# Kernel tuning notes

Measured on AMD Instinct MI355X. Metric: run time of the kernel, lower is better.

The kernel has to match this reference:

```python
import jax, jax.numpy as jnp
import numpy as np

E, D, A, EMB, V = 2048, 512, 512, 512, 10000  # encoder_dim, decoder_dim, attention_dim, embed_dim, vocab


def setup_inputs() -> dict:
    key = jax.random.key(0)
    ks = jax.random.split(key, 20)
    s = 0.02
    B, P, T = 64, 196, 40
    return {
        "encoder_out": jax.random.normal(ks[0], (B, P, E), jnp.float32),
        "captions": jax.random.randint(ks[1], (B, T), 0, V),
        "caption_lengths": jax.random.randint(ks[2], (B,), 1, T),
        "enc_att_W": jax.random.normal(ks[3], (E, A)) * s,
        "enc_att_b": jnp.zeros((A,)),
        "dec_att_W": jax.random.normal(ks[4], (D, A)) * s,
        "dec_att_b": jnp.zeros((A,)),
        "full_att_W": jax.random.normal(ks[5], (A,)) * s,
        "full_att_b": jnp.zeros(()),
        "embedding": jax.random.normal(ks[6], (V, EMB)) * s,
        "W_ih": jax.random.normal(ks[7], (EMB + E, 4 * D)) * s,
        "b_ih": jnp.zeros((4 * D,)),
        "W_hh": jax.random.normal(ks[8], (D, 4 * D)) * s,
        "b_hh": jnp.zeros((4 * D,)),
        "init_h_W": jax.random.normal(ks[9], (E, D)) * s,
        "init_h_b": jnp.zeros((D,)),
        "init_c_W": jax.random.normal(ks[10], (E, D)) * s,
        "init_c_b": jnp.zeros((D,)),
        "fc_W": jax.random.normal(ks[11], (D, V)) * s,
        "fc_b": jnp.zeros((V,)),
        "f_beta_W": jax.random.normal(ks[12], (D, E)) * s,
        "f_beta_b": jnp.zeros((E,)),
    }


def reference(encoder_out, captions, caption_lengths,
              enc_att_W, enc_att_b, dec_att_W, dec_att_b, full_att_W, full_att_b,
              embedding, W_ih, b_ih, W_hh, b_hh,
              init_h_W, init_h_b, init_c_W, init_c_b,
              fc_W, fc_b, f_beta_W, f_beta_b):
    # init hidden state from mean-pooled encoder features
    mean_enc = encoder_out.mean(axis=1)                      # [B, E]
    h = mean_enc @ init_h_W + init_h_b                       # [B, D]
    c = mean_enc @ init_c_W + init_c_b

    embs = embedding[captions]                               # [B, T, EMB]
    # encoder_att(encoder_out) is step-invariant -> precompute once
    att1 = jnp.einsum('bpe,ea->bpa', encoder_out, enc_att_W) + enc_att_b  # [B, P, A]

    def step(carry, emb_t):
        h, c = carry
        att2 = h @ dec_att_W + dec_att_b                     # [B, A]
        e = jax.nn.relu(att1 + att2[:, None, :]) @ full_att_W + full_att_b  # [B, P]
        alpha = jax.nn.softmax(e, axis=1)                    # [B, P]
        context = jnp.einsum('bpe,bp->be', encoder_out, alpha)  # [B, E]
        gate = jax.nn.sigmoid(h @ f_beta_W + f_beta_b)       # [B, E]
        x = jnp.concatenate([emb_t, gate * context], axis=1)  # [B, EMB+E]
        gates = x @ W_ih + b_ih + h @ W_hh + b_hh            # [B, 4D]
        i, f, g, o = jnp.split(gates, 4, axis=1)
        c_new = jax.nn.sigmoid(f) * c + jax.nn.sigmoid(i) * jnp.tanh(g)
        h_new = jax.nn.sigmoid(o) * jnp.tanh(c_new)
        preds = h_new @ fc_W + fc_b                          # [B, V] (dropout = identity at eval)
        return (h_new, c_new), (preds, alpha)

    (_, _), (preds_t, alphas_t) = jax.lax.scan(step, (h, c), jnp.swapaxes(embs, 0, 1))
    predictions = jnp.swapaxes(preds_t, 0, 1)                # [B, T, V]
    alphas = jnp.swapaxes(alphas_t, 0, 1)                    # [B, T, P]
    return predictions, alphas
```

## Files before the change

kernel.cpp:

```cpp
#include <hip/hip_runtime.h>
#include <cstdint>
#include <cstddef>

#define B_   64
#define P_   196
#define E_   2048
#define A_   512
#define D_   512
#define EMB_ 512
#define V_   10000
#define T_   40
#define NCAT  4608
#define VPAD  10112

typedef unsigned short u16;
typedef __attribute__((ext_vector_type(8))) short bf16x8;
typedef __attribute__((ext_vector_type(4))) float f32x4;

__device__ __forceinline__ f32x4 mfma_bf16(bf16x8 a, bf16x8 b, f32x4 c) {
  return __builtin_amdgcn_mfma_f32_16x16x32_bf16(a, b, c, 0, 0, 0);
}
__device__ __forceinline__ u16 f2b(float f) {
  unsigned u = __builtin_bit_cast(unsigned, f);
  u += 0x7fffu + ((u >> 16) & 1u);
  return (u16)(u >> 16);
}
__device__ __forceinline__ float b2f(u16 s) {
  unsigned u = ((unsigned)s) << 16;
  return __builtin_bit_cast(float, u);
}
__device__ __forceinline__ float sigf(float x) { return 1.0f / (1.0f + __expf(-x)); }

__device__ __forceinline__ void gl_lds16(const u16* gsrc, u16* ldst) {
  __builtin_amdgcn_global_load_lds(
      (const __attribute__((address_space(1))) unsigned int*)gsrc,
      (__attribute__((address_space(3))) unsigned int*)ldst,
      16, 0, 0);
}

__global__ __launch_bounds__(256) void k_cvt_bf16(const float* __restrict__ s,
                                                  u16* __restrict__ d, int n4) {
  int i = blockIdx.x * 256 + threadIdx.x;
  if (i >= n4) return;
  float4 v = reinterpret_cast<const float4*>(s)[i];
  u16* o = d + (size_t)i * 4;
  o[0] = f2b(v.x); o[1] = f2b(v.y); o[2] = f2b(v.z); o[3] = f2b(v.w);
}

__global__ __launch_bounds__(256) void k_mean(const float* __restrict__ enc,
                                              u16* __restrict__ meanE_bf) {
  int i = blockIdx.x * 256 + threadIdx.x;
  int b = i >> 11, e = i & 2047;
  const float* p = enc + (size_t)b * P_ * E_ + e;
  float s = 0.f;
  for (int pp = 0; pp < P_; ++pp) s += p[(size_t)pp * E_];
  meanE_bf[i] = f2b(s * (1.0f / (float)P_));
}

__global__ __launch_bounds__(256) void k_transpose_bf16(
    const float* __restrict__ src, int srcStride,
    u16* __restrict__ dst, int dstStride, int N, int K) {
  __shared__ float t[32][33];
  int kt = blockIdx.x * 32, nt = blockIdx.y * 32;
  int tx = threadIdx.x & 31, ty = threadIdx.x >> 5;
  #pragma unroll
  for (int i = 0; i < 4; ++i) {
    int k = kt + ty + i * 8, n = nt + tx;
    t[ty + i * 8][tx] = (k < K && n < N) ? src[(size_t)k * srcStride + n] : 0.0f;
  }
  __syncthreads();
  #pragma unroll
  for (int i = 0; i < 4; ++i) {
    int n = nt + ty + i * 8, k = kt + tx;
    if (n < N && k < K) dst[(size_t)n * dstStride + k] = f2b(t[tx][ty + i * 8]);
  }
}

__global__ __launch_bounds__(256) void k_emb(const int* __restrict__ captions,
                                             const float* __restrict__ embedding,
                                             u16* __restrict__ embs) {
  int i = blockIdx.x * 256 + threadIdx.x;
  int m = i >> 9, k = i & 511;
  int t = m >> 6, b = m & 63;
  int cap = captions[b * T_ + t];
  embs[i] = f2b(embedding[(size_t)cap * EMB_ + k]);
}

__global__ __launch_bounds__(256) void k_bsum(const float* __restrict__ a,
                                              const float* __restrict__ b,
                                              float* __restrict__ o) {
  int i = blockIdx.x * 256 + threadIdx.x;
  o[i] = a[i] + b[i];
}

__global__ __launch_bounds__(256) void k_catbias(const float* __restrict__ hb,
                                                 const float* __restrict__ cb,
                                                 float* __restrict__ o) {
  int i = blockIdx.x * 256 + threadIdx.x;
  o[i] = (i < 512) ? hb[i] : cb[i - 512];
}

__global__ __launch_bounds__(256) void k_hc_pack(const float* __restrict__ initHC,
                                                 u16* __restrict__ h0_bf,
                                                 float* __restrict__ c_f) {
  int i = blockIdx.x * 256 + threadIdx.x;
  int b = i >> 9, d = i & 511;
  h0_bf[i] = f2b(initHC[b * 1024 + d]);
  c_f[i]  = initHC[b * 1024 + 512 + d];
}

template <bool BF16OUT>
__global__ __launch_bounds__(256) void k_gemm_bt(
    const u16* __restrict__ Am, const u16* __restrict__ Bt,
    const float* __restrict__ bias, void* __restrict__ outp, int K, int N) {
  int m0 = blockIdx.x * 64, n0 = blockIdx.y * 64;
  int w = threadIdx.x >> 6, lane = threadIdx.x & 63;
  int lr = lane & 15, lg = lane >> 4;
  const u16* ap = Am + (size_t)(m0 + 16 * w + lr) * K + lg * 8;
  const u16* bp = Bt + (size_t)(n0 + lr) * K + lg * 8;
  f32x4 acc0 = {}, acc1 = {}, acc2 = {}, acc3 = {};
  for (int k = 0; k < K; k += 32) {
    bf16x8 a  = *reinterpret_cast<const bf16x8*>(ap + k);
    bf16x8 b0 = *reinterpret_cast<const bf16x8*>(bp + k);
    bf16x8 b1 = *reinterpret_cast<const bf16x8*>(bp + (size_t)16 * K + k);
    bf16x8 b2 = *reinterpret_cast<const bf16x8*>(bp + (size_t)32 * K + k);
    bf16x8 b3 = *reinterpret_cast<const bf16x8*>(bp + (size_t)48 * K + k);
    acc0 = mfma_bf16(a, b0, acc0);
    acc1 = mfma_bf16(a, b1, acc1);
    acc2 = mfma_bf16(a, b2, acc2);
    acc3 = mfma_bf16(a, b3, acc3);
  }
  int row = m0 + 16 * w + 4 * lg;
  f32x4 accs[4] = {acc0, acc1, acc2, acc3};
  #pragma unroll
  for (int ns = 0; ns < 4; ++ns) {
    int col = n0 + 16 * ns + lr;
    float bv = bias[col];
    #pragma unroll
    for (int r = 0; r < 4; ++r) {
      float v = accs[ns][r] + bv;
      if (BF16OUT) ((u16*)outp)[(size_t)(row + r) * N + col] = f2b(v);
      else         ((float*)outp)[(size_t)(row + r) * N + col] = v;
    }
  }
}

template <bool BF16OUT>
__global__ __launch_bounds__(256) void k_gemm128(
    const u16* __restrict__ Am, const u16* __restrict__ Bt,
    const float* __restrict__ bias, void* __restrict__ outp, int K, int N) {
  __shared__ u16 lA[128 * 64];
  __shared__ u16 lB[128 * 64];
  int n0 = blockIdx.x * 128, m0 = blockIdx.y * 128;
  int w = threadIdx.x >> 6, lane = threadIdx.x & 63;
  int wr = w >> 1, wc = w & 1;
  int lr = lane & 15, lg = lane >> 4;
  int srow = lane >> 3;
  int scol = (lane & 7) * 8;
  f32x4 acc[4][4] = {};
  for (int kt = 0; kt < K; kt += 64) {
    #pragma unroll
    for (int q = 0; q < 4; ++q) {
      int r = (w * 4 + q) * 8 + srow;
      gl_lds16(Am + (size_t)(m0 + r) * K + kt + scol, &lA[(w * 4 + q) * 512]);
      gl_lds16(Bt + (size_t)(n0 + r) * K + kt + scol, &lB[(w * 4 + q) * 512]);
    }
    __syncthreads();
    #pragma unroll
    for (int kk = 0; kk < 2; ++kk) {
      bf16x8 af[4], bf[4];
      #pragma unroll
      for (int m = 0; m < 4; ++m)
        af[m] = *reinterpret_cast<const bf16x8*>(&lA[(wr * 64 + m * 16 + lr) * 64 + kk * 32 + lg * 8]);
      #pragma unroll
      for (int n = 0; n < 4; ++n)
        bf[n] = *reinterpret_cast<const bf16x8*>(&lB[(wc * 64 + n * 16 + lr) * 64 + kk * 32 + lg * 8]);
      #pragma unroll
      for (int m = 0; m < 4; ++m)
        #pragma unroll
        for (int n = 0; n < 4; ++n)
          acc[m][n] = mfma_bf16(af[m], bf[n], acc[m][n]);
    }
    __syncthreads();
  }
  #pragma unroll
  for (int n = 0; n < 4; ++n) {
    int col = n0 + wc * 64 + n * 16 + lr;
    float bv = bias[col];
    #pragma unroll
    for (int m = 0; m < 4; ++m) {
      int row = m0 + wr * 64 + m * 16 + lg * 4;
      #pragma unroll
      for (int r = 0; r < 4; ++r) {
        float v = acc[m][n][r] + bv;
        if (BF16OUT) ((u16*)outp)[(size_t)(row + r) * N + col] = f2b(v);
        else         ((float*)outp)[(size_t)(row + r) * N + col] = v;
      }
    }
  }
}

__global__ __launch_bounds__(256) void k_gemm_fc(
    const u16* __restrict__ Hall1, const u16* __restrict__ fcWT,
    const float* __restrict__ fc_b, float* __restrict__ preds_out) {
  __shared__ u16 lA[128 * 64];
  __shared__ u16 lB[128 * 64];
  int n0 = blockIdx.x * 128, m0 = blockIdx.y * 128;
  int w = threadIdx.x >> 6, lane = threadIdx.x & 63;
  int wr = w >> 1, wc = w & 1;
  int lr = lane & 15, lg = lane >> 4;
  int srow = lane >> 3;
  int scol = (lane & 7) * 8;
  f32x4 acc[4][4] = {};
  for (int kt = 0; kt < 512; kt += 64) {
    #pragma unroll
    for (int q = 0; q < 4; ++q) {
      int r = (w * 4 + q) * 8 + srow;
      gl_lds16(Hall1 + (size_t)(m0 + r) * 512 + kt + scol, &lA[(w * 4 + q) * 512]);
      gl_lds16(fcWT + (size_t)(n0 + r) * 512 + kt + scol, &lB[(w * 4 + q) * 512]);
    }
    __syncthreads();
    #pragma unroll
    for (int kk = 0; kk < 2; ++kk) {
      bf16x8 af[4], bf[4];
      #pragma unroll
      for (int m = 0; m < 4; ++m)
        af[m] = *reinterpret_cast<const bf16x8*>(&lA[(wr * 64 + m * 16 + lr) * 64 + kk * 32 + lg * 8]);
      #pragma unroll
      for (int n = 0; n < 4; ++n)
        bf[n] = *reinterpret_cast<const bf16x8*>(&lB[(wc * 64 + n * 16 + lr) * 64 + kk * 32 + lg * 8]);
      #pragma unroll
      for (int m = 0; m < 4; ++m)
        #pragma unroll
        for (int n = 0; n < 4; ++n)
          acc[m][n] = mfma_bf16(af[m], bf[n], acc[m][n]);
    }
    __syncthreads();
  }
  #pragma unroll
  for (int n = 0; n < 4; ++n) {
    int col = n0 + wc * 64 + n * 16 + lr;
    if (col >= V_) continue;
    float bv = fc_b[col];
    #pragma unroll
    for (int m = 0; m < 4; ++m) {
      int row = m0 + wr * 64 + m * 16 + lg * 4;
      #pragma unroll
      for (int r = 0; r < 4; ++r) {
        int rr = row + r;
        int t = rr >> 6, b = rr & 63;
        preds_out[((size_t)b * T_ + t) * V_ + col] = acc[m][n][r] + bv;
      }
    }
  }
}

__global__ __launch_bounds__(256) void k_stepA(
    const u16* __restrict__ h_bf, const u16* __restrict__ catW,
    const float* __restrict__ dec_b, const float* __restrict__ fbeta_b,
    const float* __restrict__ embW_t,
    float* __restrict__ att2, float* __restrict__ gate,
    float* __restrict__ gates) {
  int n0 = blockIdx.x * 64;
  int w = threadIdx.x >> 6, lane = threadIdx.x & 63;
  int lr = lane & 15, lg = lane >> 4;
  const u16* ap = h_bf + (size_t)(16 * w + lr) * 512 + lg * 8;
  const u16* bp = catW + (size_t)(n0 + lr) * 512 + lg * 8;
  f32x4 acc0 = {}, acc1 = {}, acc2 = {}, acc3 = {};
  for (int k = 0; k < 512; k += 32) {
    bf16x8 a  = *reinterpret_cast<const bf16x8*>(ap + k);
    bf16x8 b0 = *reinterpret_cast<const bf16x8*>(bp + k);
    bf16x8 b1 = *reinterpret_cast<const bf16x8*>(bp + (size_t)16 * 512 + k);
    bf16x8 b2 = *reinterpret_cast<const bf16x8*>(bp + (size_t)32 * 512 + k);
    bf16x8 b3 = *reinterpret_cast<const bf16x8*>(bp + (size_t)48 * 512 + k);
    acc0 = mfma_bf16(a, b0, acc0);
    acc1 = mfma_bf16(a, b1, acc1);
    acc2 = mfma_bf16(a, b2, acc2);
    acc3 = mfma_bf16(a, b3, acc3);
  }
  int brow = 16 * w + 4 * lg;
  f32x4 accs[4] = {acc0, acc1, acc2, acc3};
  #pragma unroll
  for (int ns = 0; ns < 4; ++ns) {
    int n = n0 + 16 * ns + lr;
    #pragma unroll
    for (int r = 0; r < 4; ++r) {
      int b = brow + r;
      float v = accs[ns][r];
      if (n < 512) {
        att2[b * 512 + n] = v + dec_b[n];
      } else if (n < 2560) {
        int j = n - 512;
        gate[b * 2048 + j] = sigf(v + fbeta_b[j]);
      } else {
        int j = n - 2560;
        gates[b * 2048 + j] = v + embW_t[b * 2048 + j];
      }
    }
  }
}

__global__ __launch_bounds__(256) void k_stepB(
    const u16* __restrict__ att1, const float* __restrict__ att2,
    const float* __restrict__ wf, const float* __restrict__ bf_,
    float* __restrict__ e) {
  int unit = blockIdx.x * 4 + (threadIdx.x >> 6);
  int lane = threadIdx.x & 63;
  int b = unit / 196;
  const u16*  a1  = att1 + (size_t)unit * 512 + lane * 8;
  const float* a2 = att2 + b * 512 + lane * 8;
  const float* wv = wf + lane * 8;
  float s = 0.f;
  #pragma unroll
  for (int j = 0; j < 8; ++j) {
    float x = b2f(a1[j]) + a2[j];
    s += fmaxf(x, 0.f) * wv[j];
  }
  #pragma unroll
  for (int off = 32; off > 0; off >>= 1) s += __shfl_xor(s, off);
  if (lane == 0) e[unit] = s + bf_[0];
}

__global__ __launch_bounds__(256) void k_stepD(
    const float* __restrict__ e, const u16* __restrict__ enc_bf,
    const float* __restrict__ gate, float* __restrict__ alphas,
    u16* __restrict__ gctx) {
  __shared__ float sal[P_];
  __shared__ float red[256];
  int b = blockIdx.x >> 3, ch = blockIdx.x & 7;
  int tid = threadIdx.x;
  float ev = (tid < P_) ? e[b * P_ + tid] : -1e30f;
  red[tid] = ev; __syncthreads();
  for (int s = 128; s > 0; s >>= 1) {
    if (tid < s) red[tid] = fmaxf(red[tid], red[tid + s]);
    __syncthreads();
  }
  float mx = red[0]; __syncthreads();
  float ex = (tid < P_) ? __expf(ev - mx) : 0.f;
  red[tid] = ex; __syncthreads();
  for (int s = 128; s > 0; s >>= 1) {
    if (tid < s) red[tid] += red[tid + s];
    __syncthreads();
  }
  float inv = 1.0f / red[0];
  if (tid < P_) {
    float al = ex * inv;
    sal[tid] = al;
    if (ch == 0) alphas[(size_t)b * (T_ * P_) + tid] = al;
  }
  __syncthreads();
  int eidx = ch * 256 + tid;
  const u16* ep = enc_bf + (size_t)b * P_ * E_ + eidx;
  float acc = 0.f;
  #pragma unroll 4
  for (int p = 0; p < P_; ++p) acc += sal[p] * b2f(ep[(size_t)p * E_]);
  gctx[b * E_ + eidx] = f2b(acc * gate[b * E_ + eidx]);
}

__global__ __launch_bounds__(256) void k_stepE1(
    const u16* __restrict__ gctx, const u16* __restrict__ Wt,
    float* __restrict__ gates) {
  int n0 = (blockIdx.x & 31) * 64;
  int k0 = (blockIdx.x >> 5) * 256;
  int w = threadIdx.x >> 6, lane = threadIdx.x & 63;
  int lr = lane & 15, lg = lane >> 4;
  const u16* ap = gctx + (size_t)(16 * w + lr) * 2048 + lg * 8 + k0;
  const u16* bp = Wt + (size_t)(n0 + lr) * 2048 + lg * 8 + k0;
  f32x4 acc0 = {}, acc1 = {}, acc2 = {}, acc3 = {};
  for (int k = 0; k < 256; k += 32) {
    bf16x8 a  = *reinterpret_cast<const bf16x8*>(ap + k);
    bf16x8 b0 = *reinterpret_cast<const bf16x8*>(bp + k);
    bf16x8 b1 = *reinterpret_cast<const bf16x8*>(bp + (size_t)16 * 2048 + k);
    bf16x8 b2 = *reinterpret_cast<const bf16x8*>(bp + (size_t)32 * 2048 + k);
    bf16x8 b3 = *reinterpret_cast<const bf16x8*>(bp + (size_t)48 * 2048 + k);
    acc0 = mfma_bf16(a, b0, acc0);
    acc1 = mfma_bf16(a, b1, acc1);
    acc2 = mfma_bf16(a, b2, acc2);
    acc3 = mfma_bf16(a, b3, acc3);
  }
  int brow = 16 * w + 4 * lg;
  f32x4 accs[4] = {acc0, acc1, acc2, acc3};
  #pragma unroll
  for (int ns = 0; ns < 4; ++ns) {
    int n = n0 + 16 * ns + lr;
    #pragma unroll
    for (int r = 0; r < 4; ++r)
      atomicAdd(&gates[(brow + r) * 2048 + n], accs[ns][r]);
  }
}

__global__ __launch_bounds__(256) void k_stepE2(
    const float* __restrict__ gates, float* __restrict__ c, u16* __restrict__ h_out) {
  int i = blockIdx.x * 256 + threadIdx.x;
  int b = i >> 9, d = i & 511;
  const float* g = gates + (size_t)b * 2048;
  float gi = g[d], gf = g[d + 512], gg = g[d + 1024], go = g[d + 1536];
  float cn = sigf(gf) * c[i] + sigf(gi) * tanhf(gg);
  float hn = sigf(go) * tanhf(cn);
  c[i] = cn;
  h_out[i] = f2b(hn);
}

extern "C" void kernel_launch(void* const* d_in, const int* in_sizes, int n_in,
                              void* d_out, int out_size, void* d_ws, size_t ws_size,
                              hipStream_t stream) {
  (void)in_sizes; (void)n_in; (void)out_size;
  const float* enc        = (const float*)d_in[0];
  const int*   captions   = (const int*)d_in[1];
  const float* enc_att_W  = (const float*)d_in[3];
  const float* enc_att_b  = (const float*)d_in[4];
  const float* dec_att_W  = (const float*)d_in[5];
  const float* dec_att_b  = (const float*)d_in[6];
  const float* full_att_W = (const float*)d_in[7];
  const float* full_att_b = (const float*)d_in[8];
  const float* embedding  = (const float*)d_in[9];
  const float* W_ih       = (const float*)d_in[10];
  const float* b_ih       = (const float*)d_in[11];
  const float* W_hh       = (const float*)d_in[12];
  const float* b_hh       = (const float*)d_in[13];
  const float* init_h_W   = (const float*)d_in[14];
  const float* init_h_b   = (const float*)d_in[15];
  const float* init_c_W   = (const float*)d_in[16];
  const float* init_c_b   = (const float*)d_in[17];
  const float* fc_W       = (const float*)d_in[18];
  const float* fc_b       = (const float*)d_in[19];
  const float* f_beta_W   = (const float*)d_in[20];
  const float* f_beta_b   = (const float*)d_in[21];

  float* preds_out  = (float*)d_out;
  float* alphas_out = (float*)d_out + (size_t)B_ * T_ * V_;

  char* w = (char*)d_ws;
  auto alloc = [&](size_t bytes) -> char* {
    char* p = w; w += (bytes + 255) & ~(size_t)255; return p;
  };
  u16*   enc_bf   = (u16*)  alloc((size_t)B_ * P_ * E_ * 2);
  u16*   att1_bf  = (u16*)  alloc((size_t)B_ * P_ * A_ * 2);
  u16*   catW     = (u16*)  alloc((size_t)NCAT * 512 * 2);
  u16*   fcWT     = (u16*)  alloc((size_t)VPAD * 512 * 2);
  u16*   encattWT = (u16*)  alloc((size_t)A_ * E_ * 2);
  u16*   WihembT  = (u16*)  alloc((size_t)2048 * 512 * 2);
  u16*   Wih2T    = (u16*)  alloc((size_t)2048 * 2048 * 2);
  u16*   embs_bf  = (u16*)  alloc((size_t)T_ * B_ * EMB_ * 2);
  float* embW     = (float*)alloc((size_t)T_ * B_ * 2048 * 4);
  u16*   Hall     = (u16*)  alloc((size_t)(T_ + 1) * B_ * D_ * 2);
  u16*   catInit  = (u16*)  alloc((size_t)1024 * 2048 * 2);
  float* catInitB = (float*)alloc(1024 * 4);
  float* initHC   = (float*)alloc((size_t)B_ * 1024 * 4);
  u16*   meanE_bf = (u16*)  alloc((size_t)B_ * E_ * 2);
  float* c_f      = (float*)alloc((size_t)B_ * D_ * 4);
  float* att2_f   = (float*)alloc((size_t)B_ * A_ * 4);
  float* gate_f   = (float*)alloc((size_t)B_ * E_ * 4);
  float* gates_f  = (float*)alloc((size_t)B_ * 2048 * 4);
  float* e_f      = (float*)alloc((size_t)B_ * P_ * 4);
  u16*   gctx_bf  = (u16*)  alloc((size_t)B_ * E_ * 2);
  float* bsum     = (float*)alloc(2048 * 4);
  if ((size_t)(w - (char*)d_ws) > ws_size) return;

  k_cvt_bf16<<<25088, 256, 0, stream>>>(enc, enc_bf, (B_ * P_ * E_) / 4);
  k_mean<<<512, 256, 0, stream>>>(enc, meanE_bf);
  k_transpose_bf16<<<dim3(16, 16), 256, 0, stream>>>(dec_att_W, 512, catW, 512, 512, 512);
  k_transpose_bf16<<<dim3(16, 64), 256, 0, stream>>>(f_beta_W, 2048, catW + (size_t)512 * 512, 512, 2048, 512);
  k_transpose_bf16<<<dim3(16, 64), 256, 0, stream>>>(W_hh, 2048, catW + (size_t)2560 * 512, 512, 2048, 512);
  hipMemsetAsync(fcWT + (size_t)V_ * 512, 0, (size_t)(VPAD - V_) * 512 * 2, stream);
  k_transpose_bf16<<<dim3(16, 313), 256, 0, stream>>>(fc_W, 10000, fcWT, 512, 10000, 512);
  k_transpose_bf16<<<dim3(64, 16), 256, 0, stream>>>(enc_att_W, 512, encattWT, 2048, 512, 2048);
  k_transpose_bf16<<<dim3(16, 64), 256, 0, stream>>>(W_ih, 2048, WihembT, 512, 2048, 512);
  k_transpose_bf16<<<dim3(64, 64), 256, 0, stream>>>(W_ih + (size_t)512 * 2048, 2048, Wih2T, 2048, 2048, 2048);
  k_transpose_bf16<<<dim3(64, 16), 256, 0, stream>>>(init_h_W, 512, catInit, 2048, 512, 2048);
  k_transpose_bf16<<<dim3(64, 16), 256, 0, stream>>>(init_c_W, 512, catInit + (size_t)512 * 2048, 2048, 512, 2048);
  k_catbias<<<4, 256, 0, stream>>>(init_h_b, init_c_b, catInitB);
  k_bsum<<<8, 256, 0, stream>>>(b_ih, b_hh, bsum);
  k_emb<<<5120, 256, 0, stream>>>(captions, embedding, embs_bf);
  k_gemm_bt<false><<<dim3(1, 16), 256, 0, stream>>>(meanE_bf, catInit, catInitB, initHC, 2048, 1024);
  k_hc_pack<<<128, 256, 0, stream>>>(initHC, Hall, c_f);
  k_gemm128<true><<<dim3(4, 98), 256, 0, stream>>>(enc_bf, encattWT, enc_att_b, att1_bf, 2048, 512);
  k_gemm128<false><<<dim3(16, 20), 256, 0, stream>>>(embs_bf, WihembT, bsum, embW, 512, 2048);

  for (int t = 0; t < T_; ++t) {
    const u16* h_prev = Hall + (size_t)t * B_ * D_;
    u16* h_next = Hall + (size_t)(t + 1) * B_ * D_;
    k_stepA<<<NCAT / 64, 256, 0, stream>>>(h_prev, catW, dec_att_b, f_beta_b,
                                           embW + (size_t)t * B_ * 2048,
                                           att2_f, gate_f, gates_f);
    k_stepB<<<3136, 256, 0, stream>>>(att1_bf, att2_f, full_att_W, full_att_b, e_f);
    k_stepD<<<512, 256, 0, stream>>>(e_f, enc_bf, gate_f, alphas_out + (size_t)t * P_, gctx_bf);
    k_stepE1<<<256, 256, 0, stream>>>(gctx_bf, Wih2T, gates_f);
    k_stepE2<<<128, 256, 0, stream>>>(gates_f, c_f, h_next);
  }
  k_gemm_fc<<<dim3(VPAD / 128, (T_ * B_) / 128), 256, 0, stream>>>(
      Hall + (size_t)B_ * D_, fcWT, fc_b, preds_out);
}
```

Before: 2.555 ms.

## Fuse recurrent step kernels into one persistent kernel with grid barriers

Replaces the 200 per-timestep kernel launches (five kernels times forty steps) with a single persistent kernel of 256 blocks. Blocks synchronise through an atomic-counter grid barrier between phases. The attention score and softmax stages are merged so each block handles one batch row and quarter of the context columns, dropping the intermediate score buffer. This removes launch overhead and inter-kernel gaps, but relies on all 256 blocks being co-resident and adds spin-wait cost; the spin timeout could silently break correctness if residency fails.

Measured after the change: 9.889 ms. +287.1%, slower.

```diff
diff --git a/kernel.cpp b/kernel.cpp
--- a/kernel.cpp
+++ b/kernel.cpp
@@ -12,6 +12,7 @@
 #define T_   40
 #define NCAT  4608
 #define VPAD  10112
+#define NBLK  256
 
 typedef unsigned short u16;
 typedef __attribute__((ext_vector_type(8))) short bf16x8;
@@ -36,6 +37,21 @@
       (const __attribute__((address_space(1))) unsigned int*)gsrc,
       (__attribute__((address_space(3))) unsigned int*)ldst,
       16, 0, 0);
+}
+
+__device__ __forceinline__ void gbar(unsigned* bar, unsigned target) {
+  __syncthreads();
+  if (threadIdx.x == 0) {
+    __threadfence();
+    __hip_atomic_fetch_add(bar, 1u, __ATOMIC_RELEASE, __HIP_MEMORY_SCOPE_AGENT);
+    long spins = 0;
+    while (__hip_atomic_load(bar, __ATOMIC_ACQUIRE, __HIP_MEMORY_SCOPE_AGENT) < target) {
+      __builtin_amdgcn_s_sleep(8);
+      if (++spins > (1L << 19)) break;
+    }
+    __threadfence();
+  }
+  __syncthreads();
 }
 
 __global__ __launch_bounds__(256) void k_cvt_bf16(const float* __restrict__ s,
@@ -255,150 +271,174 @@
   }
 }
 
-__global__ __launch_bounds__(256) void k_stepA(
-    const u16* __restrict__ h_bf, const u16* __restrict__ catW,
-    const float* __restrict__ dec_b, const float* __restrict__ fbeta_b,
-    const float* __restrict__ embW_t,
-    float* __restrict__ att2, float* __restrict__ gate,
-    float* __restrict__ gates) {
-  int n0 = blockIdx.x * 64;
-  int w = threadIdx.x >> 6, lane = threadIdx.x & 63;
+struct LoopArgs {
+  const u16* catW;
+  const u16* att1;
+  const u16* enc;
+  const u16* Wih2T;
+  const float* embW;
+  u16* Hall;
+  float* c;
+  float* att2;
+  float* gate;
+  float* gates;
+  u16* gctx;
+  float* alphas;
+  const float* dec_b;
+  const float* fbeta_b;
+  const float* wf;
+  const float* fab;
+  unsigned* bar;
+};
+
+__global__ __launch_bounds__(256, 1) void k_loop(LoopArgs a) {
+  __shared__ float sal[256];
+  __shared__ float red[256];
+  int blk = blockIdx.x, tid = threadIdx.x;
+  int w = tid >> 6, lane = tid & 63;
   int lr = lane & 15, lg = lane >> 4;
-  const u16* ap = h_bf + (size_t)(16 * w + lr) * 512 + lg * 8;
-  const u16* bp = catW + (size_t)(n0 + lr) * 512 + lg * 8;
-  f32x4 acc0 = {}, acc1 = {}, acc2 = {}, acc3 = {};
-  for (int k = 0; k < 512; k += 32) {
-    bf16x8 a  = *reinterpret_cast<const bf16x8*>(ap + k);
-    bf16x8 b0 = *reinterpret_cast<const bf16x8*>(bp + k);
-    bf16x8 b1 = *reinterpret_cast<const bf16x8*>(bp + (size_t)16 * 512 + k);
-    bf16x8 b2 = *reinterpret_cast<const bf16x8*>(bp + (size_t)32 * 512 + k);
-    bf16x8 b3 = *reinterpret_cast<const bf16x8*>(bp + (size_t)48 * 512 + k);
-    acc0 = mfma_bf16(a, b0, acc0);
-    acc1 = mfma_bf16(a, b1, acc1);
-    acc2 = mfma_bf16(a, b2, acc2);
-    acc3 = mfma_bf16(a, b3, acc3);
-  }
-  int brow = 16 * w + 4 * lg;
-  f32x4 accs[4] = {acc0, acc1, acc2, acc3};
-  #pragma unroll
-  for (int ns = 0; ns < 4; ++ns) {
-    int n = n0 + 16 * ns + lr;
-    #pragma unroll
-    for (int r = 0; r < 4; ++r) {
-      int b = brow + r;
-      float v = accs[ns][r];
-      if (n < 512) {
-        att2[b * 512 + n] = v + dec_b[n];
-      } else if (n < 2560) {
-        int j = n - 512;
-        gate[b * 2048 + j] = sigf(v + fbeta_b[j]);
-      } else {
-        int j = n - 2560;
-        gates[b * 2048 + j] = v + embW_t[b * 2048 + j];
-      }
-    }
-  }
-}
-
-__global__ __launch_bounds__(256) void k_stepB(
-    const u16* __restrict__ att1, const float* __restrict__ att2,
-    const float* __restrict__ wf, const float* __restrict__ bf_,
-    float* __restrict__ e) {
-  int unit = blockIdx.x * 4 + (threadIdx.x >> 6);
-  int lane = threadIdx.x & 63;
-  int b = unit / 196;
-  const u16*  a1  = att1 + (size_t)unit * 512 + lane * 8;
-  const float* a2 = att2 + b * 512 + lane * 8;
-  const float* wv = wf + lane * 8;
-  float s = 0.f;
-  #pragma unroll
-  for (int j = 0; j < 8; ++j) {
-    float x = b2f(a1[j]) + a2[j];
-    s += fmaxf(x, 0.f) * wv[j];
-  }
-  #pragma unroll
-  for (int off = 32; off > 0; off >>= 1) s += __shfl_xor(s, off);
-  if (lane == 0) e[unit] = s + bf_[0];
-}
-
-__global__ __launch_bounds__(256) void k_stepD(
-    const float* __restrict__ e, const u16* __restrict__ enc_bf,
-    const float* __restrict__ gate, float* __restrict__ alphas,
-    u16* __restrict__ gctx) {
-  __shared__ float sal[P_];
-  __shared__ float red[256];
-  int b = blockIdx.x >> 3, ch = blockIdx.x & 7;
-  int tid = threadIdx.x;
-  float ev = (tid < P_) ? e[b * P_ + tid] : -1e30f;
-  red[tid] = ev; __syncthreads();
-  for (int s = 128; s > 0; s >>= 1) {
-    if (tid < s) red[tid] = fmaxf(red[tid], red[tid + s]);
-    __syncthreads();
-  }
-  float mx = red[0]; __syncthreads();
-  float ex = (tid < P_) ? __expf(ev - mx) : 0.f;
-  red[tid] = ex; __syncthreads();
-  for (int s = 128; s > 0; s >>= 1) {
-    if (tid < s) red[tid] += red[tid + s];
-    __syncthreads();
-  }
-  float inv = 1.0f / red[0];
-  if (tid < P_) {
-    float al = ex * inv;
-    sal[tid] = al;
-    if (ch == 0) alphas[(size_t)b * (T_ * P_) + tid] = al;
-  }
-  __syncthreads();
-  int eidx = ch * 256 + tid;
-  const u16* ep = enc_bf + (size_t)b * P_ * E_ + eidx;
-  float acc = 0.f;
-  #pragma unroll 4
-  for (int p = 0; p < P_; ++p) acc += sal[p] * b2f(ep[(size_t)p * E_]);
-  gctx[b * E_ + eidx] = f2b(acc * gate[b * E_ + eidx]);
-}
-
-__global__ __launch_bounds__(256) void k_stepE1(
-    const u16* __restrict__ gctx, const u16* __restrict__ Wt,
-    float* __restrict__ gates) {
-  int n0 = (blockIdx.x & 31) * 64;
-  int k0 = (blockIdx.x >> 5) * 256;
-  int w = threadIdx.x >> 6, lane = threadIdx.x & 63;
-  int lr = lane & 15, lg = lane >> 4;
-  const u16* ap = gctx + (size_t)(16 * w + lr) * 2048 + lg * 8 + k0;
-  const u16* bp = Wt + (size_t)(n0 + lr) * 2048 + lg * 8 + k0;
-  f32x4 acc0 = {}, acc1 = {}, acc2 = {}, acc3 = {};
-  for (int k = 0; k < 256; k += 32) {
-    bf16x8 a  = *reinterpret_cast<const bf16x8*>(ap + k);
-    bf16x8 b0 = *reinterpret_cast<const bf16x8*>(bp + k);
-    bf16x8 b1 = *reinterpret_cast<const bf16x8*>(bp + (size_t)16 * 2048 + k);
-    bf16x8 b2 = *reinterpret_cast<const bf16x8*>(bp + (size_t)32 * 2048 + k);
-    bf16x8 b3 = *reinterpret_cast<const bf16x8*>(bp + (size_t)48 * 2048 + k);
-    acc0 = mfma_bf16(a, b0, acc0);
-    acc1 = mfma_bf16(a, b1, acc1);
-    acc2 = mfma_bf16(a, b2, acc2);
-    acc3 = mfma_bf16(a, b3, acc3);
-  }
-  int brow = 16 * w + 4 * lg;
-  f32x4 accs[4] = {acc0, acc1, acc2, acc3};
-  #pragma unroll
-  for (int ns = 0; ns < 4; ++ns) {
-    int n = n0 + 16 * ns + lr;
-    #pragma unroll
-    for (int r = 0; r < 4; ++r)
-      atomicAdd(&gates[(brow + r) * 2048 + n], accs[ns][r]);
-  }
-}
-
-__global__ __launch_bounds__(256) void k_stepE2(
-    const float* __restrict__ gates, float* __restrict__ c, u16* __restrict__ h_out) {
-  int i = blockIdx.x * 256 + threadIdx.x;
-  int b = i >> 9, d = i & 511;
-  const float* g = gates + (size_t)b * 2048;
-  float gi = g[d], gf = g[d + 512], gg = g[d + 1024], go = g[d + 1536];
-  float cn = sigf(gf) * c[i] + sigf(gi) * tanhf(gg);
-  float hn = sigf(go) * tanhf(cn);
-  c[i] = cn;
-  h_out[i] = f2b(hn);
+  unsigned gen = 0;
+
+  for (int t = 0; t < T_; ++t) {
+    const u16* h = a.Hall + (size_t)t * B_ * D_;
+    if (blk < NCAT / 64) {
+      int n0 = blk * 64;
+      const u16* ap = h + (size_t)(16 * w + lr) * 512 + lg * 8;
+      const u16* bp = a.catW + (size_t)(n0 + lr) * 512 + lg * 8;
+      f32x4 acc0 = {}, acc1 = {}, acc2 = {}, acc3 = {};
+      for (int k = 0; k < 512; k += 32) {
+        bf16x8 av  = *reinterpret_cast<const bf16x8*>(ap + k);
+        bf16x8 b0 = *reinterpret_cast<const bf16x8*>(bp + k);
+        bf16x8 b1 = *reinterpret_cast<const bf16x8*>(bp + (size_t)16 * 512 + k);
+        bf16x8 b2 = *reinterpret_cast<const bf16x8*>(bp + (size_t)32 * 512 + k);
+        bf16x8 b3 = *reinterpret_cast<const bf16x8*>(bp + (size_t)48 * 512 + k);
+        acc0 = mfma_bf16(av, b0, acc0);
+        acc1 = mfma_bf16(av, b1, acc1);
+        acc2 = mfma_bf16(av, b2, acc2);
+        acc3 = mfma_bf16(av, b3, acc3);
+      }
+      int brow = 16 * w + 4 * lg;
+      f32x4 accs[4] = {acc0, acc1, acc2, acc3};
+      const float* embW_t = a.embW + (size_t)t * B_ * 2048;
+      #pragma unroll
+      for (int ns = 0; ns < 4; ++ns) {
+        int n = n0 + 16 * ns + lr;
+        #pragma unroll
+        for (int r = 0; r < 4; ++r) {
+          int b = brow + r;
+          float v = accs[ns][r];
+          if (n < 512) {
+            a.att2[b * 512 + n] = v + a.dec_b[n];
+          } else if (n < 2560) {
+            int j = n - 512;
+            a.gate[b * 2048 + j] = sigf(v + a.fbeta_b[j]);
+          } else {
+            int j = n - 2560;
+            a.gates[b * 2048 + j] = v + embW_t[b * 2048 + j];
+          }
+        }
+      }
+    }
+    gbar(a.bar, (++gen) * NBLK);
+
+    {
+      int b = blk >> 2, q = blk & 3;
+      float av[8], wvr[8];
+      #pragma unroll
+      for (int j = 0; j < 8; ++j) {
+        av[j]  = a.att2[b * 512 + lane * 8 + j];
+        wvr[j] = a.wf[lane * 8 + j];
+      }
+      float fb = a.fab[0];
+      for (int p = w; p < P_; p += 4) {
+        const u16* a1 = a.att1 + ((size_t)b * P_ + p) * 512 + lane * 8;
+        float s = 0.f;
+        #pragma unroll
+        for (int j = 0; j < 8; ++j) {
+          float x = b2f(a1[j]) + av[j];
+          s += fmaxf(x, 0.f) * wvr[j];
+        }
+        #pragma unroll
+        for (int off = 32; off > 0; off >>= 1) s += __shfl_xor(s, off);
+        if (lane == 0) sal[p] = s + fb;
+      }
+      __syncthreads();
+      float ev = (tid < P_) ? sal[tid] : -1e30f;
+      red[tid] = ev; __syncthreads();
+      for (int s2 = 128; s2 > 0; s2 >>= 1) {
+        if (tid < s2) red[tid] = fmaxf(red[tid], red[tid + s2]);
+        __syncthreads();
+      }
+      float mx = red[0]; __syncthreads();
+      float ex = (tid < P_) ? __expf(ev - mx) : 0.f;
+      red[tid] = ex; __syncthreads();
+      for (int s2 = 128; s2 > 0; s2 >>= 1) {
+        if (tid < s2) red[tid] += red[tid + s2];
+        __syncthreads();
+      }
+      float inv = 1.0f / red[0];
+      __syncthreads();
+      if (tid < P_) {
+        float al = ex * inv;
+        sal[tid] = al;
+        if (q == 0) a.alphas[((size_t)b * T_ + t) * P_ + tid] = al;
+      }
+      __syncthreads();
+      int col = q * 512 + tid;
+      const u16* ep = a.enc + (size_t)b * P_ * E_ + col;
+      float ac0 = 0.f, ac1 = 0.f;
+      #pragma unroll 4
+      for (int p = 0; p < P_; ++p) {
+        float al = sal[p];
+        ac0 += al * b2f(ep[(size_t)p * E_]);
+        ac1 += al * b2f(ep[(size_t)p * E_ + 256]);
+      }
+      a.gctx[b * E_ + col]       = f2b(ac0 * a.gate[b * E_ + col]);
+      a.gctx[b * E_ + col + 256] = f2b(ac1 * a.gate[b * E_ + col + 256]);
+    }
+    gbar(a.bar, (++gen) * NBLK);
+
+    {
+      int n0 = (blk & 31) * 64;
+      int k0 = (blk >> 5) * 256;
+      const u16* ap = a.gctx + (size_t)(16 * w + lr) * 2048 + lg * 8 + k0;
+      const u16* bp = a.Wih2T + (size_t)(n0 + lr) * 2048 + lg * 8 + k0;
+      f32x4 acc0 = {}, acc1 = {}, acc2 = {}, acc3 = {};
+      for (int k = 0; k < 256; k += 32) {
+        bf16x8 av  = *reinterpret_cast<const bf16x8*>(ap + k);
+        bf16x8 b0 = *reinterpret_cast<const bf16x8*>(bp + k);
+        bf16x8 b1 = *reinterpret_cast<const bf16x8*>(bp + (size_t)16 * 2048 + k);
+        bf16x8 b2 = *reinterpret_cast<const bf16x8*>(bp + (size_t)32 * 2048 + k);
+        bf16x8 b3 = *reinterpret_cast<const bf16x8*>(bp + (size_t)48 * 2048 + k);
+        acc0 = mfma_bf16(av, b0, acc0);
+        acc1 = mfma_bf16(av, b1, acc1);
+        acc2 = mfma_bf16(av, b2, acc2);
+        acc3 = mfma_bf16(av, b3, acc3);
+      }
+      int brow = 16 * w + 4 * lg;
+      f32x4 accs[4] = {acc0, acc1, acc2, acc3};
+      #pragma unroll
+      for (int ns = 0; ns < 4; ++ns) {
+        int n = n0 + 16 * ns + lr;
+        #pragma unroll
+        for (int r = 0; r < 4; ++r)
+          atomicAdd(&a.gates[(brow + r) * 2048 + n], accs[ns][r]);
+      }
+    }
+    gbar(a.bar, (++gen) * NBLK);
+
+    if (blk < 128) {
+      int i = blk * 256 + tid;
+      int b = i >> 9, d = i & 511;
+      const float* g = a.gates + (size_t)b * 2048;
+      float gi = g[d], gf = g[d + 512], gg = g[d + 1024], go = g[d + 1536];
+      float cn = sigf(gf) * a.c[i] + sigf(gi) * tanhf(gg);
+      float hn = sigf(go) * tanhf(cn);
+      a.c[i] = cn;
+      a.Hall[(size_t)(t + 1) * B_ * D_ + i] = f2b(hn);
+    }
+    gbar(a.bar, (++gen) * NBLK);
+  }
 }
 
 extern "C" void kernel_launch(void* const* d_in, const int* in_sizes, int n_in,
@@ -452,11 +492,12 @@
   float* att2_f   = (float*)alloc((size_t)B_ * A_ * 4);
   float* gate_f   = (float*)alloc((size_t)B_ * E_ * 4);
   float* gates_f  = (float*)alloc((size_t)B_ * 2048 * 4);
-  float* e_f      = (float*)alloc((size_t)B_ * P_ * 4);
   u16*   gctx_bf  = (u16*)  alloc((size_t)B_ * E_ * 2);
   float* bsum     = (float*)alloc(2048 * 4);
+  unsigned* bar   = (unsigned*)alloc(256);
   if ((size_t)(w - (char*)d_ws) > ws_size) return;
 
+  hipMemsetAsync(bar, 0, 4, stream);
   k_cvt_bf16<<<25088, 256, 0, stream>>>(enc, enc_bf, (B_ * P_ * E_) / 4);
   k_mean<<<512, 256, 0, stream>>>(enc, meanE_bf);
   k_transpose_bf16<<<dim3(16, 16), 256, 0, stream>>>(dec_att_W, 512, catW, 512, 512, 512);
@@ -477,17 +518,14 @@
   k_gemm128<true><<<dim3(4, 98), 256, 0, stream>>>(enc_bf, encattWT, enc_att_b, att1_bf, 2048, 512);
   k_gemm128<false><<<dim3(16, 20), 256, 0, stream>>>(embs_bf, WihembT, bsum, embW, 512, 2048);
 
-  for (int t = 0; t < T_; ++t) {
-    const u16* h_prev = Hall + (size_t)t * B_ * D_;
-    u16* h_next = Hall + (size_t)(t + 1) * B_ * D_;
-    k_stepA<<<NCAT / 64, 256, 0, stream>>>(h_prev, catW, dec_att_b, f_beta_b,
-                                           embW + (size_t)t * B_ * 2048,
-                                           att2_f, gate_f, gates_f);
-    k_stepB<<<3136, 256, 0, stream>>>(att1_bf, att2_f, full_att_W, full_att_b, e_f);
-    k_stepD<<<512, 256, 0, stream>>>(e_f, enc_bf, gate_f, alphas_out + (size_t)t * P_, gctx_bf);
-    k_stepE1<<<256, 256, 0, stream>>>(gctx_bf, Wih2T, gates_f);
-    k_stepE2<<<128, 256, 0, stream>>>(gates_f, c_f, h_next);
-  }
+  LoopArgs la;
+  la.catW = catW; la.att1 = att1_bf; la.enc = enc_bf; la.Wih2T = Wih2T;
+  la.embW = embW; la.Hall = Hall; la.c = c_f; la.att2 = att2_f;
+  la.gate = gate_f; la.gates = gates_f; la.gctx = gctx_bf; la.alphas = alphas_out;
+  la.dec_b = dec_att_b; la.fbeta_b = f_beta_b; la.wf = full_att_W; la.fab = full_att_b;
+  la.bar = bar;
+  k_loop<<<NBLK, 256, 0, stream>>>(la);
+
   k_gemm_fc<<<dim3(VPAD / 128, (T_ * B_) / 128), 256, 0, stream>>>(
       Hall + (size_t)B_ * D_, fcWT, fc_b, preds_out);
 }
```
